# Optimization experiments

Hardware: AMD Instinct MI355X
Metric: run time of the kernel (lower is better)

## Reference

```python
import jax, jax.numpy as jnp
import numpy as np

BATCH, NUM_FEAT, EMB = 1024, 32, 16
HIDDEN = [128, 128, 128]


def setup_inputs() -> dict:
    key = jax.random.key(0)
    ks = jax.random.split(key, 4)
    inputs = jax.random.normal(ks[0], (BATCH, NUM_FEAT, EMB), dtype=jnp.float32)
    # Conv1D kernel_size=1 -> dense weight of shape (in_dim, units) per layer.
    # in_dim_i = h_{i-1} * num_feat, with h_{-1} = num_feat.
    in0 = NUM_FEAT * NUM_FEAT          # 1024
    in1 = HIDDEN[0] * NUM_FEAT         # 4096
    in2 = HIDDEN[1] * NUM_FEAT         # 4096
    scale = lambda fan_in: (1.0 / np.sqrt(fan_in)).astype(np.float32) if isinstance(fan_in, np.ndarray) else np.float32(1.0 / np.sqrt(fan_in))
    W0 = jax.random.normal(ks[1], (in0, HIDDEN[0]), dtype=jnp.float32) * scale(in0)
    W1 = jax.random.normal(ks[2], (in1, HIDDEN[1]), dtype=jnp.float32) * scale(in1)
    W2 = jax.random.normal(ks[3], (in2, HIDDEN[2]), dtype=jnp.float32) * scale(in2)
    b0 = jnp.zeros((HIDDEN[0],), dtype=jnp.float32)
    b1 = jnp.zeros((HIDDEN[1],), dtype=jnp.float32)
    b2 = jnp.zeros((HIDDEN[2],), dtype=jnp.float32)
    return {"inputs": inputs, "W0": W0, "b0": b0, "W1": W1, "b1": b1, "W2": W2, "b2": b2}


def reference(inputs, W0, b0, W1, b1, W2, b2):
    # inputs: (b, m, e) -> x0: (b, e, m)  [channels-last like tf.transpose perm=[0,2,1]]
    x0 = jnp.transpose(inputs, (0, 2, 1))
    b, d, m = x0.shape
    params = [(W0, b0), (W1, b1), (W2, b2)]
    xl = x0
    layer_outs = []
    for i, (W, bias) in enumerate(params):
        h = xl.shape[-1]
        # outer product over feature axes: (b, d, h, m) -> flatten to (b, d, h*m)
        zl = jnp.einsum('bdh,bdm->bdhm', xl, x0).reshape(b, d, h * m)
        xl = zl @ W + bias  # 1x1 conv == per-position GEMM
        if i < len(params) - 1:
            xl = jax.nn.relu(xl)
        layer_outs.append(xl)
    # sum over embedding axis d, concat over layers -> (b, sum(HIDDEN))
    return jnp.concatenate([o.sum(axis=1) for o in layer_outs], axis=1)
```

## Files before the change

### kernel.cpp

```cpp
#include <hip/hip_runtime.h>


typedef unsigned int u32;
typedef __attribute__((ext_vector_type(8))) short short8;
typedef __attribute__((ext_vector_type(4))) float f32x4;
typedef __attribute__((ext_vector_type(4))) u32 u32x4;

#define R_TOTAL 16384

union PackU { u32 u[4]; short8 s; };
union PackB { u32x4 v; short8 s; };

__device__ __forceinline__ u32 pack_rne(float a, float b) {
  u32 r;
  asm("v_cvt_pk_bf16_f32 %0, %1, %2" : "=v"(r) : "v"(a), "v"(b));
  return r;
}

__device__ __forceinline__ void build_x0t_body(const float* __restrict__ in,
                                               float* __restrict__ x0t,
                                               int bid, int tid, float* t) {
  const int b0 = bid * 8;
  #pragma unroll
  for (int rep = 0; rep < 4; ++rep) {
    int idx = tid + rep * 256;
    *(float4*)&t[idx * 4] = *(const float4*)&in[(size_t)b0 * 512 + idx * 4];
  }
  __syncthreads();
  #pragma unroll
  for (int rep = 0; rep < 4; ++rep) {
    int idx = tid + rep * 256;
    int m = idx >> 5, rem = idx & 31;
    int bl = rem >> 2, dq = rem & 3;
    *(float4*)&x0t[(size_t)m * R_TOTAL + (b0 + bl) * 16 + dq * 4] =
        *(const float4*)&t[bl * 512 + m * 16 + dq * 4];
  }
}

__device__ __forceinline__ void swizzle_body(const float* __restrict__ W,
                                             u32* __restrict__ wt,
                                             int bid, int tid, float* wl) {
  const int t = bid >> 2, nq = bid & 3;
  {
    int kk = tid >> 3, c4 = tid & 7;
    float4 v = *(const float4*)&W[(size_t)(t * 32 + kk) * 128 + nq * 32 + c4 * 4];
    wl[kk * 33 + c4 * 4 + 0] = v.x;
    wl[kk * 33 + c4 * 4 + 1] = v.y;
    wl[kk * 33 + c4 * 4 + 2] = v.z;
    wl[kk * 33 + c4 * 4 + 3] = v.w;
  }
  __syncthreads();
  if (tid < 128) {
    int nl = tid >> 2, p = tid & 3;
    int q = p ^ (nl & 3);
    u32 o[4];
    #pragma unroll
    for (int jj = 0; jj < 4; ++jj)
      o[jj] = pack_rne(wl[(q * 8 + 2 * jj + 0) * 33 + nl],
                       wl[(q * 8 + 2 * jj + 1) * 33 + nl]);
    *(u32x4*)(wt + (size_t)(t * 4 + nq) * 512 + nl * 16 + p * 4) =
        u32x4{o[0], o[1], o[2], o[3]};
  }
}

__global__ __launch_bounds__(256) void prep_all(
    const float* __restrict__ in, float* __restrict__ x0t,
    const float* __restrict__ W0, u32* __restrict__ wt0,
    const float* __restrict__ W1, u32* __restrict__ wt1,
    const float* __restrict__ W2, u32* __restrict__ wt2) {
  __shared__ float sh[4096];
  const int b = blockIdx.x, tid = threadIdx.x;
  if (b < 128)      build_x0t_body(in, x0t, b, tid, sh);
  else if (b < 256) swizzle_body(W0, wt0, b - 128, tid, sh);
  else if (b < 768) swizzle_body(W1, wt1, b - 256, tid, sh);
  else              swizzle_body(W2, wt2, b - 768, tid, sh);
}

#define KITER(I, SLOT, DO_ISSUE, BP)                                           \
  {                                                                            \
    f32x4 Y0[4], Y1[4];                                                        \
    _Pragma("unroll")                                                          \
    for (int f = 0; f < 4; ++f)                                                \
      Y0[f] = __builtin_amdgcn_mfma_f32_16x16x32_bf16(Ah[f].s, BP[0].s, zero4, 0, 0, 0); \
    _Pragma("unroll")                                                          \
    for (int f = 0; f < 4; ++f)                                                \
      Y1[f] = __builtin_amdgcn_mfma_f32_16x16x32_bf16(Ah[f].s, BP[1].s, zero4, 0, 0, 0); \
    _Pragma("unroll")                                                          \
    for (int f = 0; f < 4; ++f) {                                              \
      acc[f][0] += xn[SLOT][f] * Y0[f];                                        \
      acc[f][1] += xn[SLOT][f] * Y1[f];                                        \
    }                                                                          \
    if (DO_ISSUE) {                                                            \
      const u32* ib = wt + (size_t)((t0 + (I) + 2) * 4 + nq) * 512;            \
      BP[0].v = *(const u32x4*)(ib + boff0);                                   \
      BP[1].v = *(const u32x4*)(ib + boff1);                                   \
      const float* xp = xt + (size_t)(t0 + (I) + 2) * R_TOTAL + r0;            \
      xn[SLOT][0] = *(const f32x4*)(xp + 0 + q * 4);                           \
      xn[SLOT][1] = *(const f32x4*)(xp + 16 + q * 4);                          \
      xn[SLOT][2] = *(const f32x4*)(xp + 32 + q * 4);                          \
      xn[SLOT][3] = *(const f32x4*)(xp + 48 + q * 4);                          \
    }                                                                          \
  }

template <int NT, bool RELU, bool STORE_X>
__global__ __launch_bounds__(512, 2) void layer_mfma(
    const float* __restrict__ xt,
    const float* __restrict__ x0t,
    const u32* __restrict__ wt,
    const float* __restrict__ bias,
    float* __restrict__ xoutT,
    float* __restrict__ osum)
{
  constexpr int HT = NT / 2;
  static_assert((HT & 1) == 0 && HT >= 4, "pair-loop needs even HT >= 4");
  __shared__ u32 smem[16384];

  const int tid = threadIdx.x;
  const int w = tid >> 6, lane = tid & 63;
  const int ln15 = lane & 15, q = lane >> 4;
  const int kh = w & 1, nq = w >> 1;
  const int r0 = blockIdx.x * 64;
  const int sw = ln15 & 3;
  u32* mybuf = smem + w * 2048;

  const int boff0 = ln15 * 16 + ((q ^ sw) * 4);
  const int boff1 = (16 + ln15) * 16 + ((q ^ sw) * 4);

  PackU Ah[4];
  #pragma unroll
  for (int f = 0; f < 4; ++f) {
    const int rbase = r0 + f * 16 + ln15;
    float e[8];
    #pragma unroll
    for (int j = 0; j < 8; ++j) e[j] = x0t[(size_t)(q * 8 + j) * R_TOTAL + rbase];
    #pragma unroll
    for (int jj = 0; jj < 4; ++jj)
      Ah[f].u[jj] = pack_rne(e[2 * jj], e[2 * jj + 1]);
  }

  f32x4 acc[4][2];
  #pragma unroll
  for (int f = 0; f < 4; ++f)
    #pragma unroll
    for (int c = 0; c < 2; ++c) acc[f][c] = f32x4{0.f, 0.f, 0.f, 0.f};
  const f32x4 zero4 = {0.f, 0.f, 0.f, 0.f};

  const int t0 = kh * HT;

  PackB ba[2], bb[2];
  f32x4 xn[2][4];
  {
    const u32* ib = wt + (size_t)(t0 * 4 + nq) * 512;
    ba[0].v = *(const u32x4*)(ib + boff0);
    ba[1].v = *(const u32x4*)(ib + boff1);
    const float* xp = xt + (size_t)t0 * R_TOTAL + r0;
    xn[0][0] = *(const f32x4*)(xp + 0 + q * 4);
    xn[0][1] = *(const f32x4*)(xp + 16 + q * 4);
    xn[0][2] = *(const f32x4*)(xp + 32 + q * 4);
    xn[0][3] = *(const f32x4*)(xp + 48 + q * 4);
  }
  {
    const u32* ib = wt + (size_t)((t0 + 1) * 4 + nq) * 512;
    bb[0].v = *(const u32x4*)(ib + boff0);
    bb[1].v = *(const u32x4*)(ib + boff1);
    const float* xp = xt + (size_t)(t0 + 1) * R_TOTAL + r0;
    xn[1][0] = *(const f32x4*)(xp + 0 + q * 4);
    xn[1][1] = *(const f32x4*)(xp + 16 + q * 4);
    xn[1][2] = *(const f32x4*)(xp + 32 + q * 4);
    xn[1][3] = *(const f32x4*)(xp + 48 + q * 4);
  }

  for (int i = 0; i < HT - 2; i += 2) {
    KITER(i,     0, 1, ba);
    KITER(i + 1, 1, 1, bb);
  }
  KITER(HT - 2, 0, 0, ba);
  KITER(HT - 1, 1, 0, bb);

  __syncthreads();
  if (kh == 1) {
    u32* reg = mybuf;
    #pragma unroll
    for (int f = 0; f < 4; ++f)
      #pragma unroll
      for (int c = 0; c < 2; ++c)
        *(f32x4*)(reg + ((size_t)(f * 2 + c) * 64 + lane) * 4) = acc[f][c];
  }
  __syncthreads();
  if (kh == 0) {
    const u32* reg = smem + (w + 1) * 2048;
    float bs[2];
    #pragma unroll
    for (int c = 0; c < 2; ++c) bs[c] = bias[nq * 32 + c * 16 + ln15];

    f32x4 vv[4][2];
    #pragma unroll
    for (int f = 0; f < 4; ++f) {
      #pragma unroll
      for (int c = 0; c < 2; ++c) {
        f32x4 part = *(const f32x4*)(reg + ((size_t)(f * 2 + c) * 64 + lane) * 4);
        f32x4 v = acc[f][c] + part;
        v.x += bs[c]; v.y += bs[c]; v.z += bs[c]; v.w += bs[c];
        if (RELU) {
          v.x = fmaxf(v.x, 0.f); v.y = fmaxf(v.y, 0.f);
          v.z = fmaxf(v.z, 0.f); v.w = fmaxf(v.w, 0.f);
        }
        vv[f][c] = v;
        float s = v.x + v.y + v.z + v.w;
        s += __shfl_xor(s, 16, 64);
        s += __shfl_xor(s, 32, 64);
        if (q == 0)
          osum[(size_t)((r0 >> 4) + f) * 384 + nq * 32 + c * 16 + ln15] = s;
      }
    }

    if (STORE_X) {
      u32* myreg = mybuf;
      #pragma unroll
      for (int f = 0; f < 4; ++f)
        #pragma unroll
        for (int c = 0; c < 2; ++c)
          *(f32x4*)(myreg + ((size_t)(f * 2 + c) * 64 + lane) * 4) = vv[f][c];
      #pragma unroll
      for (int c = 0; c < 2; ++c) {
        #pragma unroll
        for (int s = 0; s < 4; ++s) {
          f32x4 vr = *(const f32x4*)(myreg +
              ((size_t)(s * 2 + c) * 64 + (lane & 3) * 16 + (lane >> 2)) * 4);
          const int col = nq * 32 + c * 16 + (lane >> 2);
          *(f32x4*)&xoutT[(size_t)col * R_TOTAL + r0 + s * 16 + (lane & 3) * 4] = vr;
        }
      }
    }
  }
}

extern "C" void kernel_launch(void* const* d_in, const int* in_sizes, int n_in,
                              void* d_out, int out_size, void* d_ws, size_t ws_size,
                              hipStream_t stream) {
  const float* in = (const float*)d_in[0];
  const float* W0 = (const float*)d_in[1];
  const float* b0 = (const float*)d_in[2];
  const float* W1 = (const float*)d_in[3];
  const float* b1 = (const float*)d_in[4];
  const float* W2 = (const float*)d_in[5];
  const float* b2 = (const float*)d_in[6];
  float* out = (float*)d_out;

  float* X0T = (float*)d_ws;
  float* X1T = X0T + (size_t)32 * R_TOTAL;
  float* X2T = X1T + (size_t)128 * R_TOTAL;
  u32* Wt0 = (u32*)(X2T + (size_t)128 * R_TOTAL);
  u32* Wt1 = Wt0 + (size_t)32 * 4 * 512;
  u32* Wt2 = Wt1 + (size_t)128 * 4 * 512;

  prep_all<<<1280, 256, 0, stream>>>(in, X0T, W0, Wt0, W1, Wt1, W2, Wt2);

  layer_mfma<32, true, true><<<256, 512, 0, stream>>>(X0T, X0T, Wt0, b0, X1T, out + 0);
  layer_mfma<128, true, true><<<256, 512, 0, stream>>>(X1T, X0T, Wt1, b1, X2T, out + 128);
  layer_mfma<128, false, false><<<256, 512, 0, stream>>>(X2T, X0T, Wt2, b2, nullptr, out + 256);
}
```

Baseline: 133.5 us.

## Split layer work across N-halves per block and 4-way K split per block

Each block now covers only half of the output columns for its 64-row tile and doubles the grid to 512 blocks. Within a block the 8 waves become 2 column groups times 4 K-splits instead of 4 times 2, and partial sums are reduced through shared memory from three waves. Launch bounds rise to 4 blocks per CU, and the first MFMA batch's accumulation is interleaved before the second. The aim is more parallelism and occupancy on a small grid, in exchange for duplicated A-fragment setup and x loads across the two column halves and a larger reduction step.

```diff
diff --git a/kernel.cpp b/kernel.cpp
--- a/kernel.cpp
+++ b/kernel.cpp
@@ -83,15 +83,18 @@
     for (int f = 0; f < 4; ++f)                                                \
       Y0[f] = __builtin_amdgcn_mfma_f32_16x16x32_bf16(Ah[f].s, BP[0].s, zero4, 0, 0, 0); \
     _Pragma("unroll")                                                          \
+    for (int f = 0; f < 4; ++f) {                                              \
+      acc[f][0] += xn[SLOT][f] * Y0[f];                                        \
+    }                                                                          \
+    _Pragma("unroll")                                                          \
     for (int f = 0; f < 4; ++f)                                                \
       Y1[f] = __builtin_amdgcn_mfma_f32_16x16x32_bf16(Ah[f].s, BP[1].s, zero4, 0, 0, 0); \
     _Pragma("unroll")                                                          \
     for (int f = 0; f < 4; ++f) {                                              \
-      acc[f][0] += xn[SLOT][f] * Y0[f];                                        \
       acc[f][1] += xn[SLOT][f] * Y1[f];                                        \
     }                                                                          \
     if (DO_ISSUE) {                                                            \
-      const u32* ib = wt + (size_t)((t0 + (I) + 2) * 4 + nq) * 512;            \
+      const u32* ib = wt + (size_t)((t0 + (I) + 2) * 4 + nqg) * 512;           \
       BP[0].v = *(const u32x4*)(ib + boff0);                                   \
       BP[1].v = *(const u32x4*)(ib + boff1);                                   \
       const float* xp = xt + (size_t)(t0 + (I) + 2) * R_TOTAL + r0;            \
@@ -103,7 +106,7 @@
   }
 
 template <int NT, bool RELU, bool STORE_X>
-__global__ __launch_bounds__(512, 2) void layer_mfma(
+__global__ __launch_bounds__(512, 4) void layer_mfma(
     const float* __restrict__ xt,
     const float* __restrict__ x0t,
     const u32* __restrict__ wt,
@@ -111,15 +114,16 @@
     float* __restrict__ xoutT,
     float* __restrict__ osum)
 {
-  constexpr int HT = NT / 2;
+  constexpr int HT = NT / 4;
   static_assert((HT & 1) == 0 && HT >= 4, "pair-loop needs even HT >= 4");
   __shared__ u32 smem[16384];
 
   const int tid = threadIdx.x;
   const int w = tid >> 6, lane = tid & 63;
   const int ln15 = lane & 15, q = lane >> 4;
-  const int kh = w & 1, nq = w >> 1;
-  const int r0 = blockIdx.x * 64;
+  const int kh = w >> 1, nq = w & 1;
+  const int r0 = (blockIdx.x >> 1) * 64;
+  const int nqg = (blockIdx.x & 1) * 2 + nq;
   const int sw = ln15 & 3;
   u32* mybuf = smem + w * 2048;
 
@@ -150,7 +154,7 @@
   PackB ba[2], bb[2];
   f32x4 xn[2][4];
   {
-    const u32* ib = wt + (size_t)(t0 * 4 + nq) * 512;
+    const u32* ib = wt + (size_t)(t0 * 4 + nqg) * 512;
     ba[0].v = *(const u32x4*)(ib + boff0);
     ba[1].v = *(const u32x4*)(ib + boff1);
     const float* xp = xt + (size_t)t0 * R_TOTAL + r0;
@@ -160,7 +164,7 @@
     xn[0][3] = *(const f32x4*)(xp + 48 + q * 4);
   }
   {
-    const u32* ib = wt + (size_t)((t0 + 1) * 4 + nq) * 512;
+    const u32* ib = wt + (size_t)((t0 + 1) * 4 + nqg) * 512;
     bb[0].v = *(const u32x4*)(ib + boff0);
     bb[1].v = *(const u32x4*)(ib + boff1);
     const float* xp = xt + (size_t)(t0 + 1) * R_TOTAL + r0;
@@ -178,7 +182,7 @@
   KITER(HT - 1, 1, 0, bb);
 
   __syncthreads();
-  if (kh == 1) {
+  if (kh != 0) {
     u32* reg = mybuf;
     #pragma unroll
     for (int f = 0; f < 4; ++f)
@@ -188,18 +192,21 @@
   }
   __syncthreads();
   if (kh == 0) {
-    const u32* reg = smem + (w + 1) * 2048;
     float bs[2];
     #pragma unroll
-    for (int c = 0; c < 2; ++c) bs[c] = bias[nq * 32 + c * 16 + ln15];
+    for (int c = 0; c < 2; ++c) bs[c] = bias[nqg * 32 + c * 16 + ln15];
 
     f32x4 vv[4][2];
     #pragma unroll
     for (int f = 0; f < 4; ++f) {
       #pragma unroll
       for (int c = 0; c < 2; ++c) {
-        f32x4 part = *(const f32x4*)(reg + ((size_t)(f * 2 + c) * 64 + lane) * 4);
-        f32x4 v = acc[f][c] + part;
+        f32x4 v = acc[f][c];
+        #pragma unroll
+        for (int p = 1; p < 4; ++p) {
+          const u32* reg = smem + (size_t)(w + 2 * p) * 2048;
+          v += *(const f32x4*)(reg + ((size_t)(f * 2 + c) * 64 + lane) * 4);
+        }
         v.x += bs[c]; v.y += bs[c]; v.z += bs[c]; v.w += bs[c];
         if (RELU) {
           v.x = fmaxf(v.x, 0.f); v.y = fmaxf(v.y, 0.f);
@@ -210,7 +217,7 @@
         s += __shfl_xor(s, 16, 64);
         s += __shfl_xor(s, 32, 64);
         if (q == 0)
-          osum[(size_t)((r0 >> 4) + f) * 384 + nq * 32 + c * 16 + ln15] = s;
+          osum[(size_t)((r0 >> 4) + f) * 384 + nqg * 32 + c * 16 + ln15] = s;
       }
     }
 
@@ -227,7 +234,7 @@
         for (int s = 0; s < 4; ++s) {
           f32x4 vr = *(const f32x4*)(myreg +
               ((size_t)(s * 2 + c) * 64 + (lane & 3) * 16 + (lane >> 2)) * 4);
-          const int col = nq * 32 + c * 16 + (lane >> 2);
+          const int col = nqg * 32 + c * 16 + (lane >> 2);
           *(f32x4*)&xoutT[(size_t)col * R_TOTAL + r0 + s * 16 + (lane & 3) * 4] = vr;
         }
       }
@@ -256,7 +263,7 @@
 
   prep_all<<<1280, 256, 0, stream>>>(in, X0T, W0, Wt0, W1, Wt1, W2, Wt2);
 
-  layer_mfma<32, true, true><<<256, 512, 0, stream>>>(X0T, X0T, Wt0, b0, X1T, out + 0);
-  layer_mfma<128, true, true><<<256, 512, 0, stream>>>(X1T, X0T, Wt1, b1, X2T, out + 128);
-  layer_mfma<128, false, false><<<256, 512, 0, stream>>>(X2T, X0T, Wt2, b2, nullptr, out + 256);
-}
+  layer_mfma<32, true, true><<<512, 512, 0, stream>>>(X0T, X0T, Wt0, b0, X1T, out + 0);
+  layer_mfma<128, true, true><<<512, 512, 0, stream>>>(X1T, X0T, Wt1, b1, X2T, out + 128);
+  layer_mfma<128, false, false><<<512, 512, 0, stream>>>(X2T, X0T, Wt2, b2, nullptr, out + 256);
+}
```

Measured after the change: 142.7 us. 1.07x slower.
